# Kernel optimization log

Hardware: AMD Instinct MI355X
Metric: run time of the kernel (lower is better)

Reference implementation:

```python
import jax, jax.numpy as jnp
import numpy as np

ALPHA = 0.2        # LeakyReLU negative slope (config['alpha'])
NEG_INF = -9e15    # mask value from the original code


def setup_inputs() -> dict:
    key = jax.random.key(0)
    k1, k2, k3, k4 = jax.random.split(key, 4)
    N, Fin, Fout = 8192, 512, 256
    inp = jax.random.normal(k1, (N, Fin), dtype=jnp.float32)
    adj = jax.random.randint(k2, (N, N), 0, 2, dtype=jnp.int32)
    # xavier_uniform with gain=1.414
    limW = 1.414 * np.sqrt(6.0 / (Fin + Fout))
    W = jax.random.uniform(k3, (Fin, Fout), dtype=jnp.float32, minval=-limW, maxval=limW)
    lima = 1.414 * np.sqrt(6.0 / (2 * Fout + 1))
    a = jax.random.uniform(k4, (2 * Fout, 1), dtype=jnp.float32, minval=-lima, maxval=lima)
    return {"input": inp, "adj": adj, "W": W, "a": a}


def reference(input, adj, W, a):
    # h: [N, F]
    h = input @ W
    Fout = W.shape[1]
    # The original builds a_input[i, j] = concat(h_i, h_j) and dots with a.
    # Equivalently: e_ij = leakyrelu(h_i . a[:F] + h_j . a[F:]), computed
    # without the O(N^2 * 2F) intermediate.
    s1 = h @ a[:Fout, 0]   # [N] contribution from node i
    s2 = h @ a[Fout:, 0]   # [N] contribution from node j
    e = s1[:, None] + s2[None, :]                     # [N, N]
    e = jnp.where(e > 0, e, ALPHA * e)                # LeakyReLU
    scores = jnp.where(adj > 0, e, NEG_INF)
    attention = jax.nn.softmax(scores, axis=1)        # row-wise softmax
    # dropout is identity in inference mode (training=False)
    h_prime = attention @ h                           # [N, F]
    return jax.nn.elu(h_prime)                        # concat=True path
```

## Files before the change

kernel.cpp:

```cpp
#include <hip/hip_runtime.h>
#include <stdint.h>
#include <stddef.h>


#define N_NODES 8192
#define FIN     512
#define FOUT    256
#define LRALPHA 0.2f
#define MI_SHIFT 16.0f

typedef float f32x4 __attribute__((ext_vector_type(4)));
typedef short s16x8 __attribute__((ext_vector_type(8)));
typedef unsigned short u16x4 __attribute__((ext_vector_type(4)));
typedef int   i32x4 __attribute__((ext_vector_type(4)));
typedef unsigned long long u64;

__device__ __forceinline__ short f2bf_rne(float f) {
  uint32_t u = __builtin_bit_cast(uint32_t, f);
  u += 0x7fffu + ((u >> 16) & 1u);
  return (short)(u >> 16);
}
__device__ __forceinline__ short f2bf_fast(float f) {
  uint32_t u = __builtin_bit_cast(uint32_t, f);
  return (short)((u + 0x8000u) >> 16);
}
__device__ __forceinline__ float bf2f(short s) {
  uint32_t u = ((uint32_t)(uint16_t)s) << 16;
  return __builtin_bit_cast(float, u);
}

__global__ __launch_bounds__(256) void k_prep(const float* __restrict__ W,
                                              uint16_t* __restrict__ WThi,
                                              uint16_t* __restrict__ WTlo) {
  const int idx = blockIdx.x * 256 + threadIdx.x;
  const int n = idx >> 9;
  const int k = idx & 511;
  float v = W[k * FOUT + n];
  short h = f2bf_rne(v);
  WThi[idx] = (uint16_t)h;
  WTlo[idx] = (uint16_t)f2bf_rne(v - bf2f(h));
}

__global__ __launch_bounds__(256, 4) void k_gemm(const float* __restrict__ X,
                                                 const uint16_t* __restrict__ WThi,
                                                 const uint16_t* __restrict__ WTlo,
                                                 const float* __restrict__ a,
                                                 uint16_t* __restrict__ HTf,
                                                 float* __restrict__ s1g,
                                                 float* __restrict__ s2g) {
  __shared__ float ls1[16], ls2[16];
  __shared__ uint16_t tile[FOUT * 16];
  const int lane = threadIdx.x & 63;
  const int w    = threadIdx.x >> 6;
  const int m    = lane & 15;
  const int quad = lane >> 4;
  const int i0   = blockIdx.x * 16;
  const int colg = w * 64;

  f32x4 acc[4];
#pragma unroll
  for (int cb = 0; cb < 4; ++cb) { f32x4 z = {0.f,0.f,0.f,0.f}; acc[cb] = z; }

  for (int kt = 0; kt < FIN / 32; ++kt) {
    const int k0 = kt * 32 + quad * 8;
    const float* ap = X + (size_t)(i0 + m) * FIN + k0;
    f32x4 a0 = *(const f32x4*)ap;
    f32x4 a1 = *(const f32x4*)(ap + 4);
    s16x8 ahi, alo;
#pragma unroll
    for (int e = 0; e < 4; ++e) {
      short h0 = f2bf_rne(a0[e]); ahi[e] = h0; alo[e] = f2bf_rne(a0[e] - bf2f(h0));
      short h1 = f2bf_rne(a1[e]); ahi[4+e] = h1; alo[4+e] = f2bf_rne(a1[e] - bf2f(h1));
    }
#pragma unroll
    for (int cb = 0; cb < 4; ++cb) {
      const int n = colg + cb * 16 + m;
      s16x8 bhi = *(const s16x8*)(WThi + (size_t)n * FIN + k0);
      s16x8 blo = *(const s16x8*)(WTlo + (size_t)n * FIN + k0);
      acc[cb] = __builtin_amdgcn_mfma_f32_16x16x32_bf16(ahi, bhi, acc[cb], 0, 0, 0);
      acc[cb] = __builtin_amdgcn_mfma_f32_16x16x32_bf16(ahi, blo, acc[cb], 0, 0, 0);
      acc[cb] = __builtin_amdgcn_mfma_f32_16x16x32_bf16(alo, bhi, acc[cb], 0, 0, 0);
    }
  }

  float p1[4] = {0.f,0.f,0.f,0.f}, p2[4] = {0.f,0.f,0.f,0.f};
#pragma unroll
  for (int cb = 0; cb < 4; ++cb) {
    const int n = colg + cb * 16 + m;
    const float a1c = a[n];
    const float a2c = a[FOUT + n];
#pragma unroll
    for (int reg = 0; reg < 4; ++reg) {
      p1[reg] += acc[cb][reg] * a1c;
      p2[reg] += acc[cb][reg] * a2c;
    }
  }
#pragma unroll
  for (int off = 1; off <= 8; off <<= 1)
#pragma unroll
    for (int reg = 0; reg < 4; ++reg) {
      p1[reg] += __shfl_xor(p1[reg], off);
      p2[reg] += __shfl_xor(p2[reg], off);
    }
  if (threadIdx.x < 16) { ls1[threadIdx.x] = 0.f; ls2[threadIdx.x] = 0.f; }
  __syncthreads();
  if (m == 0) {
#pragma unroll
    for (int reg = 0; reg < 4; ++reg) {
      atomicAdd(&ls1[quad * 4 + reg], p1[reg]);
      atomicAdd(&ls2[quad * 4 + reg], p2[reg]);
    }
  }
#pragma unroll
  for (int cb = 0; cb < 4; ++cb) {
    const int col = colg + cb * 16 + m;
    u16x4 pk;
#pragma unroll
    for (int reg = 0; reg < 4; ++reg) pk[reg] = (uint16_t)f2bf_rne(acc[cb][reg]);
    *(u16x4*)(tile + col * 16 + quad * 4) = pk;
  }
  __syncthreads();
  const int t = threadIdx.x;
  if (t < 16) { s1g[i0 + t] = ls1[t]; s2g[i0 + t] = ls2[t]; }
  const int jt = i0 >> 5;
  const int qh = (i0 >> 4) & 1;
  const int c  = t >> 4;
  const int mm = t & 15;
#pragma unroll
  for (int qq = 0; qq < 2; ++qq) {
    uint4 v = *(const uint4*)(tile + (c * 16 + mm) * 16 + qq * 8);
    *(uint4*)(HTf + ((((size_t)jt * 16 + c) * 64) + (qh * 2 + qq) * 16 + mm) * 8) = v;
  }
}

__global__ __launch_bounds__(1024, 4) void k_attn(const int* __restrict__ adj,
                                                  const uint16_t* __restrict__ HTf,
                                                  const float* __restrict__ s1,
                                                  const float* __restrict__ s2,
                                                  float* __restrict__ pout,
                                                  float* __restrict__ pden,
                                                  int split) {
  __shared__ uint16_t PL[2][128 * 40];
  __shared__ float lss2[1024];

  const int tid  = threadIdx.x;
  const int lane = tid & 63;
  const int w    = tid >> 6;
  const int m    = lane & 15;
  const int q    = lane >> 4;
  const int rg   = w >> 2, cg = w & 3;
  const int pr   = tid >> 3;
  const int cpr  = tid & 7;
  const int i0   = blockIdx.x * 128;
  const int sp   = blockIdx.y;
  const int jrange = N_NODES / split;
  const int jbeg   = sp * jrange;
  const int nphase = jrange / 32;

  const float s1r = s1[i0 + pr];
  const float mi = fmaxf(s1r + MI_SHIFT, LRALPHA * (s1r + MI_SHIFT));

  f32x4 acc[2][4];
#pragma unroll
  for (int rt = 0; rt < 2; ++rt)
#pragma unroll
    for (int cb = 0; cb < 4; ++cb) { f32x4 z = {0.f,0.f,0.f,0.f}; acc[rt][cb] = z; }
  float den = 0.f;

  const int* arow = adj + (size_t)(i0 + pr) * N_NODES + jbeg + cpr * 4;
  i32x4 A_cur = *(const i32x4*)arow;
  i32x4 A_nxt = *(const i32x4*)(arow + ((1 < nphase) ? 32 : 0));

#pragma unroll 1
  for (int p = 0; p < nphase; ++p) {
    if ((p & 31) == 0) {
      __syncthreads();
      if (tid < 256) *(f32x4*)(lss2 + tid * 4) =
        *(const f32x4*)(s2 + jbeg + (p >> 5) * 1024 + tid * 4);
      __syncthreads();
    }
    const uint16_t* hB = HTf + ((size_t)((jbeg >> 5) + p) * 16 + cg * 4) * 512 + lane * 8;
    s16x8 Bv[4];
#pragma unroll
    for (int cb = 0; cb < 4; ++cb)
      Bv[cb] = *(const s16x8*)(hB + cb * 512);
    const int pn = (p + 2 < nphase) ? p + 2 : p;
    i32x4 A_pf = *(const i32x4*)(arow + pn * 32);
    const int pl = p & 31;
    f32x4 sA = *(const f32x4*)(lss2 + pl * 32 + cpr * 4);
    u16x4 P0;
#pragma unroll
    for (int e = 0; e < 4; ++e) {
      float x = s1r + sA[e];
      float pv = __expf(fmaxf(x, LRALPHA * x) - mi);
      pv = (A_cur[e] != 0) ? pv : 0.f;
      den += pv;
      P0[e] = (uint16_t)f2bf_fast(pv);
    }
    *(u16x4*)(PL[p & 1] + pr * 40 + cpr * 4) = P0;
    A_cur = A_nxt; A_nxt = A_pf;
    __syncthreads();
    s16x8 F[2];
#pragma unroll
    for (int rt = 0; rt < 2; ++rt)
      F[rt] = *(const s16x8*)(PL[p & 1] + (rg * 32 + rt * 16 + m) * 40 + q * 8);
#pragma unroll
    for (int rt = 0; rt < 2; ++rt)
#pragma unroll
      for (int cb = 0; cb < 4; ++cb)
        acc[rt][cb] = __builtin_amdgcn_mfma_f32_16x16x32_bf16(F[rt], Bv[cb], acc[rt][cb], 0, 0, 0);
  }

  den += __shfl_xor(den, 1);
  den += __shfl_xor(den, 2);
  den += __shfl_xor(den, 4);
  if (cpr == 0) pden[(size_t)sp * N_NODES + i0 + pr] = den;
#pragma unroll
  for (int rt = 0; rt < 2; ++rt)
#pragma unroll
    for (int cb = 0; cb < 4; ++cb)
#pragma unroll
      for (int reg = 0; reg < 4; ++reg) {
        const int row = i0 + rg * 32 + rt * 16 + q * 4 + reg;
        const int col = cg * 64 + cb * 16 + m;
        pout[((size_t)sp * N_NODES + row) * FOUT + col] = acc[rt][cb][reg];
      }
}

__global__ __launch_bounds__(256) void k_reduce(const float* __restrict__ pout,
                                                const float* __restrict__ pden,
                                                float* __restrict__ out,
                                                int split) {
  const int gid = blockIdx.x * 256 + threadIdx.x;
  const int i = gid >> 6;
  const int c = (gid & 63) << 2;
  f32x4 sum = {0.f,0.f,0.f,0.f};
  float den = 0.f;
  for (int s = 0; s < split; ++s) {
    sum += *(const f32x4*)(pout + ((size_t)s * N_NODES + i) * FOUT + c);
    den += pden[(size_t)s * N_NODES + i];
  }
  const float inv = 1.0f / den;
  f32x4 r;
#pragma unroll
  for (int e = 0; e < 4; ++e) {
    float v = sum[e] * inv;
    r[e] = v > 0.f ? v : (__expf(v) - 1.0f);
  }
  *(f32x4*)(out + (size_t)i * FOUT + c) = r;
}

extern "C" void kernel_launch(void* const* d_in, const int* in_sizes, int n_in,
                              void* d_out, int out_size, void* d_ws, size_t ws_size,
                              hipStream_t stream) {
  const float* X   = (const float*)d_in[0];
  const int*   adj = (const int*)d_in[1];
  const float* W   = (const float*)d_in[2];
  const float* a   = (const float*)d_in[3];
  float* out = (float*)d_out;

  char* ws = (char*)d_ws;
  uint16_t* HTf  = (uint16_t*)ws;
  uint16_t* WThi = (uint16_t*)(ws + (4u << 20));
  uint16_t* WTlo = (uint16_t*)(ws + (4u << 20) + 262144);
  float*    s1   = (float*)(ws + (4u << 20) + 524288);
  float*    s2   = s1 + N_NODES;
  float*    pden = s2 + N_NODES;
  const size_t pout_off = (size_t)16u << 20;
  const size_t slab = (size_t)N_NODES * FOUT * sizeof(float);

  int split;
  if      (ws_size >= pout_off + 8 * slab) split = 8;
  else if (ws_size >= pout_off + 4 * slab) split = 4;
  else if (ws_size >= pout_off + 2 * slab) split = 2;
  else                                     split = 1;
  float* pout = (split == 1) ? out : (float*)(ws + pout_off);

  k_prep<<<dim3(512), dim3(256), 0, stream>>>(W, WThi, WTlo);
  k_gemm<<<dim3(N_NODES / 16), dim3(256), 0, stream>>>(X, WThi, WTlo, a, HTf, s1, s2);
  k_attn<<<dim3(N_NODES / 128, split), dim3(1024), 0, stream>>>(adj, HTf, s1, s2, pout, pden, split);
  k_reduce<<<dim3(N_NODES * FOUT / 4 / 256), dim3(256), 0, stream>>>(pout, pden, out, split);
}
```

Before: 499.7 us.

## Compute attention probabilities directly in MFMA fragment layout, dropping LDS staging

Each lane now computes the softmax numerators for exactly the A-fragment elements it feeds to the MFMA, so the probabilities go straight into registers. This removes the per-phase LDS write, the __syncthreads barrier and the LDS read. Blocks shrink to 512 threads and 64 rows, and the adjacency prefetch depth drops from two phases to one. The cost is redundant exp work: all four column-group waves of a row group compute the same probabilities, so exp and adjacency loads are duplicated fourfold.

```diff
diff --git a/kernel.cpp b/kernel.cpp
--- a/kernel.cpp
+++ b/kernel.cpp
@@ -133,14 +133,13 @@
   }
 }
 
-__global__ __launch_bounds__(1024, 4) void k_attn(const int* __restrict__ adj,
-                                                  const uint16_t* __restrict__ HTf,
-                                                  const float* __restrict__ s1,
-                                                  const float* __restrict__ s2,
-                                                  float* __restrict__ pout,
-                                                  float* __restrict__ pden,
-                                                  int split) {
-  __shared__ uint16_t PL[2][128 * 40];
+__global__ __launch_bounds__(512, 2) void k_attn(const int* __restrict__ adj,
+                                                 const uint16_t* __restrict__ HTf,
+                                                 const float* __restrict__ s1,
+                                                 const float* __restrict__ s2,
+                                                 float* __restrict__ pout,
+                                                 float* __restrict__ pden,
+                                                 int split) {
   __shared__ float lss2[1024];
 
   const int tid  = threadIdx.x;
@@ -149,27 +148,31 @@
   const int m    = lane & 15;
   const int q    = lane >> 4;
   const int rg   = w >> 2, cg = w & 3;
-  const int pr   = tid >> 3;
-  const int cpr  = tid & 7;
-  const int i0   = blockIdx.x * 128;
+  const int i0   = blockIdx.x * 64;
   const int sp   = blockIdx.y;
   const int jrange = N_NODES / split;
   const int jbeg   = sp * jrange;
   const int nphase = jrange / 32;
 
-  const float s1r = s1[i0 + pr];
-  const float mi = fmaxf(s1r + MI_SHIFT, LRALPHA * (s1r + MI_SHIFT));
+  const int r0 = i0 + rg * 32 + m;
+  const int r1 = r0 + 16;
+  const float s1r0 = s1[r0];
+  const float s1r1 = s1[r1];
+  const float mi0 = fmaxf(s1r0 + MI_SHIFT, LRALPHA * (s1r0 + MI_SHIFT));
+  const float mi1 = fmaxf(s1r1 + MI_SHIFT, LRALPHA * (s1r1 + MI_SHIFT));
 
   f32x4 acc[2][4];
 #pragma unroll
   for (int rt = 0; rt < 2; ++rt)
 #pragma unroll
     for (int cb = 0; cb < 4; ++cb) { f32x4 z = {0.f,0.f,0.f,0.f}; acc[rt][cb] = z; }
-  float den = 0.f;
-
-  const int* arow = adj + (size_t)(i0 + pr) * N_NODES + jbeg + cpr * 4;
-  i32x4 A_cur = *(const i32x4*)arow;
-  i32x4 A_nxt = *(const i32x4*)(arow + ((1 < nphase) ? 32 : 0));
+  float den0 = 0.f, den1 = 0.f;
+
+  const int* a0 = adj + (size_t)r0 * N_NODES + jbeg + q * 8;
+  const int* a1 = adj + (size_t)r1 * N_NODES + jbeg + q * 8;
+
+  i32x4 A00 = *(const i32x4*)a0, A01 = *(const i32x4*)(a0 + 4);
+  i32x4 A10 = *(const i32x4*)a1, A11 = *(const i32x4*)(a1 + 4);
 
 #pragma unroll 1
   for (int p = 0; p < nphase; ++p) {
@@ -184,37 +187,40 @@
 #pragma unroll
     for (int cb = 0; cb < 4; ++cb)
       Bv[cb] = *(const s16x8*)(hB + cb * 512);
-    const int pn = (p + 2 < nphase) ? p + 2 : p;
-    i32x4 A_pf = *(const i32x4*)(arow + pn * 32);
+    const int pn = (p + 1 < nphase) ? (p + 1) * 32 : p * 32;
+    i32x4 nA00 = *(const i32x4*)(a0 + pn), nA01 = *(const i32x4*)(a0 + pn + 4);
+    i32x4 nA10 = *(const i32x4*)(a1 + pn), nA11 = *(const i32x4*)(a1 + pn + 4);
     const int pl = p & 31;
-    f32x4 sA = *(const f32x4*)(lss2 + pl * 32 + cpr * 4);
-    u16x4 P0;
+    f32x4 sA = *(const f32x4*)(lss2 + pl * 32 + q * 8);
+    f32x4 sB = *(const f32x4*)(lss2 + pl * 32 + q * 8 + 4);
+    s16x8 F0, F1;
 #pragma unroll
     for (int e = 0; e < 4; ++e) {
-      float x = s1r + sA[e];
-      float pv = __expf(fmaxf(x, LRALPHA * x) - mi);
-      pv = (A_cur[e] != 0) ? pv : 0.f;
-      den += pv;
-      P0[e] = (uint16_t)f2bf_fast(pv);
-    }
-    *(u16x4*)(PL[p & 1] + pr * 40 + cpr * 4) = P0;
-    A_cur = A_nxt; A_nxt = A_pf;
-    __syncthreads();
-    s16x8 F[2];
-#pragma unroll
-    for (int rt = 0; rt < 2; ++rt)
-      F[rt] = *(const s16x8*)(PL[p & 1] + (rg * 32 + rt * 16 + m) * 40 + q * 8);
-#pragma unroll
-    for (int rt = 0; rt < 2; ++rt)
-#pragma unroll
-      for (int cb = 0; cb < 4; ++cb)
-        acc[rt][cb] = __builtin_amdgcn_mfma_f32_16x16x32_bf16(F[rt], Bv[cb], acc[rt][cb], 0, 0, 0);
-  }
-
-  den += __shfl_xor(den, 1);
-  den += __shfl_xor(den, 2);
-  den += __shfl_xor(den, 4);
-  if (cpr == 0) pden[(size_t)sp * N_NODES + i0 + pr] = den;
+      float x, pv;
+      x = s1r0 + sA[e]; pv = __expf(fmaxf(x, LRALPHA * x) - mi0);
+      pv = (A00[e] != 0) ? pv : 0.f; den0 += pv; F0[e] = f2bf_fast(pv);
+      x = s1r0 + sB[e]; pv = __expf(fmaxf(x, LRALPHA * x) - mi0);
+      pv = (A01[e] != 0) ? pv : 0.f; den0 += pv; F0[4 + e] = f2bf_fast(pv);
+      x = s1r1 + sA[e]; pv = __expf(fmaxf(x, LRALPHA * x) - mi1);
+      pv = (A10[e] != 0) ? pv : 0.f; den1 += pv; F1[e] = f2bf_fast(pv);
+      x = s1r1 + sB[e]; pv = __expf(fmaxf(x, LRALPHA * x) - mi1);
+      pv = (A11[e] != 0) ? pv : 0.f; den1 += pv; F1[4 + e] = f2bf_fast(pv);
+    }
+    A00 = nA00; A01 = nA01; A10 = nA10; A11 = nA11;
+#pragma unroll
+    for (int cb = 0; cb < 4; ++cb)
+      acc[0][cb] = __builtin_amdgcn_mfma_f32_16x16x32_bf16(F0, Bv[cb], acc[0][cb], 0, 0, 0);
+#pragma unroll
+    for (int cb = 0; cb < 4; ++cb)
+      acc[1][cb] = __builtin_amdgcn_mfma_f32_16x16x32_bf16(F1, Bv[cb], acc[1][cb], 0, 0, 0);
+  }
+
+  den0 += __shfl_xor(den0, 16); den0 += __shfl_xor(den0, 32);
+  den1 += __shfl_xor(den1, 16); den1 += __shfl_xor(den1, 32);
+  if (cg == 0 && q == 0) {
+    pden[(size_t)sp * N_NODES + i0 + rg * 32 + m]      = den0;
+    pden[(size_t)sp * N_NODES + i0 + rg * 32 + 16 + m] = den1;
+  }
 #pragma unroll
   for (int rt = 0; rt < 2; ++rt)
 #pragma unroll
@@ -278,6 +284,6 @@
 
   k_prep<<<dim3(512), dim3(256), 0, stream>>>(W, WThi, WTlo);
   k_gemm<<<dim3(N_NODES / 16), dim3(256), 0, stream>>>(X, WThi, WTlo, a, HTf, s1, s2);
-  k_attn<<<dim3(N_NODES / 128, split), dim3(1024), 0, stream>>>(adj, HTf, s1, s2, pout, pden, split);
+  k_attn<<<dim3(N_NODES / 64, split), dim3(512), 0, stream>>>(adj, HTf, s1, s2, pout, pden, split);
   k_reduce<<<dim3(N_NODES * FOUT / 4 / 256), dim3(256), 0, stream>>>(pout, pden, out, split);
 }
```

Result: slower. 543.1 us (+8.7%).
